# Kernel tuning notes

Hardware: AMD Instinct MI355X
Metric: run time of the kernel (lower is better)

Reference implementation:

```python
import jax, jax.numpy as jnp
import numpy as np

B, S, D, H = 4, 2048, 1024, 16
HD = D // H  # head dim = 64


def setup_inputs() -> dict:
    key = jax.random.key(0)
    k1, k2, k3 = jax.random.split(key, 3)
    scale = 1.0 / np.sqrt(D).astype(np.float32)
    x = jax.random.normal(k1, (B, S, D), dtype=jnp.float32)
    # q/k slices of nn.MultiheadAttention's in_proj (v and out_proj never
    # influence the returned values since x_t is discarded by forward)
    wq = jax.random.normal(k2, (D, D), dtype=jnp.float32) * scale
    wk = jax.random.normal(k3, (D, D), dtype=jnp.float32) * scale
    bq = jnp.zeros((D,), dtype=jnp.float32)
    bk = jnp.zeros((D,), dtype=jnp.float32)
    # 8 contiguous scale blocks of 256 tokens; last boundary == S
    scales_idx = (jnp.arange(1, 9, dtype=jnp.int64) * (S // 8))
    return {"x": x, "wq": wq, "wk": wk, "bq": bq, "bk": bk,
            "scales_idx": scales_idx}


def reference(x, wq, wk, bq, bk, scales_idx):
    b, s, d = x.shape
    # project q, k and split heads: [B, H, S, HD]
    q = (x @ wq.T + bq).reshape(b, s, H, HD).transpose(0, 2, 1, 3)
    k = (x @ wk.T + bk).reshape(b, s, H, HD).transpose(0, 2, 1, 3)
    inv_sqrt_hd = jnp.asarray(1.0 / np.sqrt(HD), dtype=x.dtype)
    scores = jnp.einsum('bhqd,bhkd->bhqk', q, k) * inv_sqrt_hd  # [B,H,S,S]
    # block-diagonal mask: token i belongs to the block whose right boundary
    # is the first scales_idx entry strictly greater than i
    pos = jnp.arange(s)
    seg = jnp.searchsorted(scales_idx, pos, side='right')  # [S]
    allowed = seg[:, None] == seg[None, :]                  # [S,S] bool
    scores = jnp.where(allowed[None, None], scores, -jnp.inf)
    w = jax.nn.softmax(scores, axis=-1)  # every row has >=1 allowed entry
    weights_attn = jnp.mean(w, axis=1)   # average over heads -> [B,S,S]
    return (x, weights_attn)
```

## Files before the change

### kernel.cpp

```cpp
#include <hip/hip_runtime.h>
#include <hip/hip_bf16.h>
#include <math.h>

#define BB 4
#define SS 2048
#define DD 1024
#define HH 16
#define HD 64
#define MM (BB*SS)
#define NN (2*DD)
#define BK 64
#define NKT 16

typedef __attribute__((ext_vector_type(8))) short short8;
typedef __attribute__((ext_vector_type(4))) float f32x4;
typedef unsigned short ushort_t;

__device__ __forceinline__ void gload16(const void* g, void* l) {
    __builtin_amdgcn_global_load_lds((const __attribute__((address_space(1))) unsigned int*)g,
                                     (__attribute__((address_space(3))) unsigned int*)l,
                                     16, 0, 0);
}

__global__ __launch_bounds__(256)
void copy_cast(const float* __restrict__ x, float* __restrict__ out_x,
               __hip_bfloat16* __restrict__ xb, int n8)
{
    int i = blockIdx.x * 256 + threadIdx.x;
    if (i >= n8) return;
    const f32x4* s = (const f32x4*)x + (size_t)i * 2;
    f32x4 a = s[0], b = s[1];
    f32x4* o = (f32x4*)out_x + (size_t)i * 2;
    __builtin_nontemporal_store(a, o);
    __builtin_nontemporal_store(b, o + 1);
    __hip_bfloat16 tmp[8];
    tmp[0] = __float2bfloat16(a.x); tmp[1] = __float2bfloat16(a.y);
    tmp[2] = __float2bfloat16(a.z); tmp[3] = __float2bfloat16(a.w);
    tmp[4] = __float2bfloat16(b.x); tmp[5] = __float2bfloat16(b.y);
    tmp[6] = __float2bfloat16(b.z); tmp[7] = __float2bfloat16(b.w);
    *(float4*)&xb[(size_t)i * 8] = *(float4*)tmp;
}

__global__ __launch_bounds__(256)
void cast_w(const float* __restrict__ wq, const float* __restrict__ wk,
            __hip_bfloat16* __restrict__ wb)
{
    const int half = (DD * DD) / 8;
    int i = blockIdx.x * 256 + threadIdx.x;
    if (i >= 2 * half) return;
    const float* src = (i < half) ? wq : wk;
    int j = (i < half) ? i : i - half;
    const float4* s = (const float4*)src + (size_t)j * 2;
    float4 a = s[0], b = s[1];
    __hip_bfloat16 tmp[8];
    tmp[0] = __float2bfloat16(a.x); tmp[1] = __float2bfloat16(a.y);
    tmp[2] = __float2bfloat16(a.z); tmp[3] = __float2bfloat16(a.w);
    tmp[4] = __float2bfloat16(b.x); tmp[5] = __float2bfloat16(b.y);
    tmp[6] = __float2bfloat16(b.z); tmp[7] = __float2bfloat16(b.w);
    *(float4*)&wb[(size_t)i * 8] = *(float4*)tmp;
}

__device__ __forceinline__ void stage_A(const ushort_t* __restrict__ xb, ushort_t* Ab,
                                        int m0, int kt, int mh, int wv, int lane)
{
    #pragma unroll
    for (int it = 0; it < 2; ++it) {
        int rl0 = it * 64 + wv * 8;
        int r0 = (rl0 & 63) + ((rl0 >> 6) << 7) + mh * 64;
        int r  = r0 + (lane >> 3);
        int gch = (lane & 7) ^ (r & 7);
        gload16(xb + (size_t)(m0 + r) * DD + kt + gch * 8, Ab + r0 * 64);
    }
}

__device__ __forceinline__ void stage_Bt(const ushort_t* __restrict__ wb, ushort_t* Bb,
                                         int n0, int kt, int nh, int wv, int lane)
{
    #pragma unroll
    for (int it = 0; it < 2; ++it) {
        int rl0 = it * 64 + wv * 8;
        int r0 = (rl0 & 31) + ((rl0 >> 5) << 6) + nh * 32;
        int r  = r0 + (lane >> 3);
        int gch = (lane & 7) ^ (r & 7);
        gload16(wb + (size_t)(n0 + r) * DD + kt + gch * 8, Bb + r0 * 64);
    }
}

__global__ __launch_bounds__(512, 2)
void proj_mfma(const ushort_t* __restrict__ xb, const ushort_t* __restrict__ wb,
               const float* __restrict__ bq, const float* __restrict__ bk,
               __hip_bfloat16* __restrict__ Qb, __hip_bfloat16* __restrict__ Kb)
{
    __shared__ __align__(16) ushort_t As[2][256 * BK];
    __shared__ __align__(16) ushort_t Bs[2][256 * BK];

    const int t = threadIdx.x;
    const int wv = t >> 6, lane = t & 63, quad = lane >> 4, l15 = lane & 15;
    const int wr = wv >> 2, wc = wv & 3;
    const int m0 = blockIdx.x * 256, n0 = blockIdx.y * 256;

    f32x4 acc[8][4];
    #pragma unroll
    for (int mt = 0; mt < 8; ++mt)
        #pragma unroll
        for (int nt = 0; nt < 4; ++nt) acc[mt][nt] = (f32x4){0.f, 0.f, 0.f, 0.f};

    stage_Bt(wb, Bs[0], n0, 0, 0, wv, lane);
    stage_A (xb, As[0], m0, 0, 0, wv, lane);
    stage_A (xb, As[0], m0, 0, 1, wv, lane);
    stage_Bt(wb, Bs[0], n0, 0, 1, wv, lane);
    stage_Bt(wb, Bs[1], n0, BK, 0, wv, lane);
    stage_A (xb, As[1], m0, BK, 0, wv, lane);
    asm volatile("s_waitcnt vmcnt(4)" ::: "memory");
    __builtin_amdgcn_s_barrier();

    #pragma unroll 1
    for (int tt = 0; tt < NKT; ++tt) {
        ushort_t* Ac = As[tt & 1];
        ushort_t* Bc = Bs[tt & 1];
        ushort_t* An = As[(tt & 1) ^ 1];
        ushort_t* Bn = Bs[(tt & 1) ^ 1];
        short8 a[8][2], b[2][2];

        #pragma unroll
        for (int mt = 0; mt < 4; ++mt)
            #pragma unroll
            for (int ks = 0; ks < 2; ++ks) {
                int r = wr * 128 + mt * 16 + l15;
                int sl = r * 8 + ((ks * 4 + quad) ^ (r & 7));
                a[mt][ks] = *(const short8*)&Ac[sl * 8];
            }
        #pragma unroll
        for (int nt = 0; nt < 2; ++nt)
            #pragma unroll
            for (int ks = 0; ks < 2; ++ks) {
                int r = wc * 64 + nt * 16 + l15;
                int sl = r * 8 + ((ks * 4 + quad) ^ (r & 7));
                b[nt][ks] = *(const short8*)&Bc[sl * 8];
            }
        if (tt + 1 < NKT) stage_A(xb, An, m0, (tt + 1) * BK, 1, wv, lane);
        __builtin_amdgcn_s_barrier();
        asm volatile("s_waitcnt lgkmcnt(0)" ::: "memory");
        __builtin_amdgcn_sched_barrier(0);
        __builtin_amdgcn_s_setprio(1);
        #pragma unroll
        for (int mt = 0; mt < 4; ++mt)
            #pragma unroll
            for (int nt = 0; nt < 2; ++nt)
                #pragma unroll
                for (int ks = 0; ks < 2; ++ks)
                    acc[mt][nt] = __builtin_amdgcn_mfma_f32_16x16x32_bf16(
                        a[mt][ks], b[nt][ks], acc[mt][nt], 0, 0, 0);
        __builtin_amdgcn_s_setprio(0);
        __builtin_amdgcn_sched_barrier(0);
        __builtin_amdgcn_s_barrier();

        #pragma unroll
        for (int mt = 0; mt < 4; ++mt)
            #pragma unroll
            for (int ks = 0; ks < 2; ++ks) {
                int r = wr * 128 + 64 + mt * 16 + l15;
                int sl = r * 8 + ((ks * 4 + quad) ^ (r & 7));
                a[4 + mt][ks] = *(const short8*)&Ac[sl * 8];
            }
        if (tt + 1 < NKT) stage_Bt(wb, Bn, n0, (tt + 1) * BK, 1, wv, lane);
        __builtin_amdgcn_s_barrier();
        asm volatile("s_waitcnt lgkmcnt(0)" ::: "memory");
        __builtin_amdgcn_sched_barrier(0);
        __builtin_amdgcn_s_setprio(1);
        #pragma unroll
        for (int mt = 0; mt < 4; ++mt)
            #pragma unroll
            for (int nt = 0; nt < 2; ++nt)
                #pragma unroll
                for (int ks = 0; ks < 2; ++ks)
                    acc[4 + mt][nt] = __builtin_amdgcn_mfma_f32_16x16x32_bf16(
                        a[4 + mt][ks], b[nt][ks], acc[4 + mt][nt], 0, 0, 0);
        __builtin_amdgcn_s_setprio(0);
        __builtin_amdgcn_sched_barrier(0);
        __builtin_amdgcn_s_barrier();

        #pragma unroll
        for (int nt = 0; nt < 2; ++nt)
            #pragma unroll
            for (int ks = 0; ks < 2; ++ks) {
                int r = wc * 64 + 32 + nt * 16 + l15;
                int sl = r * 8 + ((ks * 4 + quad) ^ (r & 7));
                b[nt][ks] = *(const short8*)&Bc[sl * 8];
            }
        if (tt + 2 < NKT) stage_Bt(wb, Bc, n0, (tt + 2) * BK, 0, wv, lane);
        __builtin_amdgcn_s_barrier();
        asm volatile("s_waitcnt lgkmcnt(0)" ::: "memory");
        __builtin_amdgcn_sched_barrier(0);
        __builtin_amdgcn_s_setprio(1);
        #pragma unroll
        for (int mt = 0; mt < 4; ++mt)
            #pragma unroll
            for (int nt = 0; nt < 2; ++nt)
                #pragma unroll
                for (int ks = 0; ks < 2; ++ks)
                    acc[mt][2 + nt] = __builtin_amdgcn_mfma_f32_16x16x32_bf16(
                        a[mt][ks], b[nt][ks], acc[mt][2 + nt], 0, 0, 0);
        __builtin_amdgcn_s_setprio(0);
        __builtin_amdgcn_sched_barrier(0);
        __builtin_amdgcn_s_barrier();

        if (tt + 2 < NKT) stage_A(xb, Ac, m0, (tt + 2) * BK, 0, wv, lane);
        __builtin_amdgcn_s_barrier();
        asm volatile("s_waitcnt lgkmcnt(0)" ::: "memory");
        __builtin_amdgcn_sched_barrier(0);
        __builtin_amdgcn_s_setprio(1);
        #pragma unroll
        for (int mt = 0; mt < 4; ++mt)
            #pragma unroll
            for (int nt = 0; nt < 2; ++nt)
                #pragma unroll
                for (int ks = 0; ks < 2; ++ks)
                    acc[4 + mt][2 + nt] = __builtin_amdgcn_mfma_f32_16x16x32_bf16(
                        a[4 + mt][ks], b[nt][ks], acc[4 + mt][2 + nt], 0, 0, 0);
        __builtin_amdgcn_s_setprio(0);
        __builtin_amdgcn_sched_barrier(0);
        if (tt < NKT - 2)       asm volatile("s_waitcnt vmcnt(4)" ::: "memory");
        else if (tt == NKT - 2) asm volatile("s_waitcnt vmcnt(0)" ::: "memory");
        __builtin_amdgcn_s_barrier();
    }

    const bool isQ = (n0 < DD);
    const float* bias = isQ ? bq : bk;
    __hip_bfloat16* outp = isQ ? Qb : Kb;
    const int nc0 = (isQ ? n0 : n0 - DD) + wc * 64;
    #pragma unroll
    for (int nt = 0; nt < 4; ++nt) {
        const int nc = nc0 + nt * 16 + l15;
        const float bv = bias[nc];
        #pragma unroll
        for (int mt = 0; mt < 8; ++mt)
            #pragma unroll
            for (int reg = 0; reg < 4; ++reg) {
                int m = m0 + wr * 128 + mt * 16 + quad * 4 + reg;
                outp[(size_t)m * DD + nc] = __float2bfloat16(acc[mt][nt][reg] + bv);
            }
    }
}

__global__ __launch_bounds__(256, 1)
void attn_block(const ushort_t* __restrict__ Qb, const ushort_t* __restrict__ Kb,
                const int* __restrict__ scales, float* __restrict__ outw)
{
    __shared__ __align__(16) char smem[147456];
    float (*comb)[256] = (float(*)[256])smem;

    const int bid = blockIdx.x;
    const int rt  = bid >> 5;
    const int blk = bid & 7, bb = (bid >> 3) & 3;
    const int start = blk ? scales[blk - 1] : 0;

    const int t = threadIdx.x;
    const int wv = t >> 6, lane = t & 63, quad = lane >> 4, l15 = lane & 15;
    const int rg = wv & 1, hg = wv >> 1;

    f32x4 accm[16];
    #pragma unroll
    for (int nt = 0; nt < 16; ++nt) accm[nt] = (f32x4){0.f, 0.f, 0.f, 0.f};

    const int qrow0 = start + rt * 32;
    const int brow  = bb * SS;

    auto stageKQ = [&](int i, int buf) {
        #pragma unroll
        for (int half = 0; half < 2; ++half) {
            const int h = half * 8 + i;
            ushort_t* Kl = (ushort_t*)(smem + (size_t)(buf * 2 + half) * 32768);
            ushort_t* Ql = (ushort_t*)(smem + 131072 + (size_t)(buf * 2 + half) * 4096);
            #pragma unroll
            for (int round = 0; round < 8; ++round) {
                int c = round * 256 + t;
                int row = c >> 3, ch = c & 7;
                int gch = ch ^ (row & 7);
                gload16(Kb + (size_t)(brow + start + row) * DD + h * HD + gch * 8,
                        Kl + ((size_t)round * 256 + wv * 64) * 8);
            }
            {
                int row = t >> 3, ch = t & 7;
                int gch = ch ^ (row & 7);
                gload16(Qb + (size_t)(brow + qrow0 + row) * DD + h * HD + gch * 8,
                        Ql + ((size_t)wv * 64) * 8);
            }
        }
    };

    stageKQ(0, 0);

    for (int i = 0; i < 8; ++i) {
        if (i < 7) {
            stageKQ(i + 1, (i + 1) & 1);
            asm volatile("s_waitcnt vmcnt(18)" ::: "memory");
        } else {
            asm volatile("s_waitcnt vmcnt(0)" ::: "memory");
        }
        __builtin_amdgcn_s_barrier();

        const ushort_t* Ks = (const ushort_t*)(smem + (size_t)((i & 1) * 2 + hg) * 32768);
        const ushort_t* Qs = (const ushort_t*)(smem + 131072 + (size_t)((i & 1) * 2 + hg) * 4096);

        short8 af[2];
        #pragma unroll
        for (int ks = 0; ks < 2; ++ks) {
            int qr = rg * 16 + l15;
            int sl = qr * 8 + ((ks * 4 + quad) ^ (qr & 7));
            af[ks] = *(const short8*)&Qs[sl * 8];
        }
        f32x4 sc[16];
        #pragma unroll
        for (int nt = 0; nt < 16; ++nt) {
            sc[nt] = (f32x4){0.f, 0.f, 0.f, 0.f};
            #pragma unroll
            for (int ks = 0; ks < 2; ++ks) {
                int kr = nt * 16 + l15;
                int sl = kr * 8 + ((ks * 4 + quad) ^ (kr & 7));
                short8 bf = *(const short8*)&Ks[sl * 8];
                sc[nt] = __builtin_amdgcn_mfma_f32_16x16x32_bf16(af[ks], bf, sc[nt], 0, 0, 0);
            }
        }
        float rs[4] = {0.f, 0.f, 0.f, 0.f};
        #pragma unroll
        for (int nt = 0; nt < 16; ++nt) {
            #pragma unroll
            for (int r = 0; r < 4; ++r) {
                float p = __expf(sc[nt][r] * 0.125f);
                sc[nt][r] = p;
                rs[r] += p;
            }
        }
        #pragma unroll
        for (int r = 0; r < 4; ++r) {
            #pragma unroll
            for (int off = 1; off < 16; off <<= 1) rs[r] += __shfl_xor(rs[r], off, 64);
            rs[r] = 1.0f / rs[r];
        }
        #pragma unroll
        for (int nt = 0; nt < 16; ++nt)
            #pragma unroll
            for (int r = 0; r < 4; ++r) accm[nt][r] += sc[nt][r] * rs[r];

        __builtin_amdgcn_s_barrier();
    }

    __syncthreads();
    if (hg == 0) {
        #pragma unroll
        for (int nt = 0; nt < 16; ++nt)
            #pragma unroll
            for (int r = 0; r < 4; ++r)
                comb[rg * 16 + quad * 4 + r][nt * 16 + l15] = accm[nt][r];
    }
    __syncthreads();
    if (hg == 1) {
        #pragma unroll
        for (int nt = 0; nt < 16; ++nt)
            #pragma unroll
            for (int r = 0; r < 4; ++r)
                comb[rg * 16 + quad * 4 + r][nt * 16 + l15] += accm[nt][r];
    }
    __syncthreads();

    const float s16 = 1.0f / (float)HH;
    const size_t orow0 = (size_t)bb * SS + qrow0;
    #pragma unroll
    for (int it = 0; it < 64; ++it) {
        int flat = it * 256 + t;
        int row = flat >> 9;
        int col = (flat & 511) * 4;
        f32x4 v = (f32x4){0.f, 0.f, 0.f, 0.f};
        unsigned lc = (unsigned)(col - start);
        if (lc < 256u) {
            const float* c = &comb[row][lc];
            v = (f32x4){c[0] * s16, c[1] * s16, c[2] * s16, c[3] * s16};
        }
        __builtin_nontemporal_store(v, (f32x4*)&outw[(orow0 + row) * SS + col]);
    }
}

extern "C" void kernel_launch(void* const* d_in, const int* in_sizes, int n_in,
                              void* d_out, int out_size, void* d_ws, size_t ws_size,
                              hipStream_t stream)
{
    const float* x  = (const float*)d_in[0];
    const float* wq = (const float*)d_in[1];
    const float* wk = (const float*)d_in[2];
    const float* bq = (const float*)d_in[3];
    const float* bk = (const float*)d_in[4];
    const int* scales = (const int*)d_in[5];

    float* out_x = (float*)d_out;
    float* out_w = out_x + (size_t)BB * SS * DD;

    char* w = (char*)d_ws;
    __hip_bfloat16* xb = (__hip_bfloat16*)(w);
    __hip_bfloat16* wb = (__hip_bfloat16*)(w + 16777216);
    __hip_bfloat16* Qb = (__hip_bfloat16*)(w + 20971520);
    __hip_bfloat16* Kb = (__hip_bfloat16*)(w + 37748736);

    copy_cast<<<4096, 256, 0, stream>>>(x, out_x, xb, (MM * DD) / 8);
    cast_w<<<1024, 256, 0, stream>>>(wq, wk, wb);

    dim3 pgrid(MM / 256, NN / 256);
    proj_mfma<<<pgrid, 512, 0, stream>>>((const ushort_t*)xb, (const ushort_t*)wb,
                                         bq, bk, Qb, Kb);

    attn_block<<<256, 256, 0, stream>>>((const ushort_t*)Qb, (const ushort_t*)Kb,
                                        scales, out_w);
}
```

Baseline: 208.0 us.

## Collapse four-phase GEMM main loop into two phases with fewer barriers

```diff
diff --git a/kernel.cpp b/kernel.cpp
--- a/kernel.cpp
+++ b/kernel.cpp
@@ -120,10 +120,10 @@
         ushort_t* Bc = Bs[tt & 1];
         ushort_t* An = As[(tt & 1) ^ 1];
         ushort_t* Bn = Bs[(tt & 1) ^ 1];
-        short8 a[8][2], b[2][2];
-
-        #pragma unroll
-        for (int mt = 0; mt < 4; ++mt)
+        short8 a[8][2], b0[2][2], b1[2][2];
+
+        #pragma unroll
+        for (int mt = 0; mt < 8; ++mt)
             #pragma unroll
             for (int ks = 0; ks < 2; ++ks) {
                 int r = wr * 128 + mt * 16 + l15;
@@ -136,88 +136,51 @@
             for (int ks = 0; ks < 2; ++ks) {
                 int r = wc * 64 + nt * 16 + l15;
                 int sl = r * 8 + ((ks * 4 + quad) ^ (r & 7));
-                b[nt][ks] = *(const short8*)&Bc[sl * 8];
-            }
-        if (tt + 1 < NKT) stage_A(xb, An, m0, (tt + 1) * BK, 1, wv, lane);
+                b0[nt][ks] = *(const short8*)&Bc[sl * 8];
+            }
+        if (tt + 1 < NKT) {
+            stage_A (xb, An, m0, (tt + 1) * BK, 1, wv, lane);
+            stage_Bt(wb, Bn, n0, (tt + 1) * BK, 1, wv, lane);
+        }
         __builtin_amdgcn_s_barrier();
         asm volatile("s_waitcnt lgkmcnt(0)" ::: "memory");
         __builtin_amdgcn_sched_barrier(0);
         __builtin_amdgcn_s_setprio(1);
         #pragma unroll
-        for (int mt = 0; mt < 4; ++mt)
+        for (int mt = 0; mt < 8; ++mt)
             #pragma unroll
             for (int nt = 0; nt < 2; ++nt)
                 #pragma unroll
                 for (int ks = 0; ks < 2; ++ks)
                     acc[mt][nt] = __builtin_amdgcn_mfma_f32_16x16x32_bf16(
-                        a[mt][ks], b[nt][ks], acc[mt][nt], 0, 0, 0);
+                        a[mt][ks], b0[nt][ks], acc[mt][nt], 0, 0, 0);
         __builtin_amdgcn_s_setprio(0);
         __builtin_amdgcn_sched_barrier(0);
         __builtin_amdgcn_s_barrier();
 
         #pragma unroll
-        for (int mt = 0; mt < 4; ++mt)
+        for (int nt = 0; nt < 2; ++nt)
             #pragma unroll
             for (int ks = 0; ks < 2; ++ks) {
-                int r = wr * 128 + 64 + mt * 16 + l15;
+                int r = wc * 64 + 32 + nt * 16 + l15;
                 int sl = r * 8 + ((ks * 4 + quad) ^ (r & 7));
-                a[4 + mt][ks] = *(const short8*)&Ac[sl * 8];
-            }
-        if (tt + 1 < NKT) stage_Bt(wb, Bn, n0, (tt + 1) * BK, 1, wv, lane);
-        __builtin_amdgcn_s_barrier();
+                b1[nt][ks] = *(const short8*)&Bc[sl * 8];
+            }
+        if (tt + 2 < NKT) {
+            stage_Bt(wb, Bc, n0, (tt + 2) * BK, 0, wv, lane);
+            stage_A (xb, Ac, m0, (tt + 2) * BK, 0, wv, lane);
+        }
         asm volatile("s_waitcnt lgkmcnt(0)" ::: "memory");
         __builtin_amdgcn_sched_barrier(0);
         __builtin_amdgcn_s_setprio(1);
         #pragma unroll
-        for (int mt = 0; mt < 4; ++mt)
-            #pragma unroll
-            for (int nt = 0; nt < 2; ++nt)
-                #pragma unroll
-                for (int ks = 0; ks < 2; ++ks)
-                    acc[4 + mt][nt] = __builtin_amdgcn_mfma_f32_16x16x32_bf16(
-                        a[4 + mt][ks], b[nt][ks], acc[4 + mt][nt], 0, 0, 0);
-        __builtin_amdgcn_s_setprio(0);
-        __builtin_amdgcn_sched_barrier(0);
-        __builtin_amdgcn_s_barrier();
-
-        #pragma unroll
-        for (int nt = 0; nt < 2; ++nt)
-            #pragma unroll
-            for (int ks = 0; ks < 2; ++ks) {
-                int r = wc * 64 + 32 + nt * 16 + l15;
-                int sl = r * 8 + ((ks * 4 + quad) ^ (r & 7));
-                b[nt][ks] = *(const short8*)&Bc[sl * 8];
-            }
-        if (tt + 2 < NKT) stage_Bt(wb, Bc, n0, (tt + 2) * BK, 0, wv, lane);
-        __builtin_amdgcn_s_barrier();
-        asm volatile("s_waitcnt lgkmcnt(0)" ::: "memory");
-        __builtin_amdgcn_sched_barrier(0);
-        __builtin_amdgcn_s_setprio(1);
-        #pragma unroll
-        for (int mt = 0; mt < 4; ++mt)
+        for (int mt = 0; mt < 8; ++mt)
             #pragma unroll
             for (int nt = 0; nt < 2; ++nt)
                 #pragma unroll
                 for (int ks = 0; ks < 2; ++ks)
                     acc[mt][2 + nt] = __builtin_amdgcn_mfma_f32_16x16x32_bf16(
-                        a[mt][ks], b[nt][ks], acc[mt][2 + nt], 0, 0, 0);
-        __builtin_amdgcn_s_setprio(0);
-        __builtin_amdgcn_sched_barrier(0);
-        __builtin_amdgcn_s_barrier();
-
-        if (tt + 2 < NKT) stage_A(xb, Ac, m0, (tt + 2) * BK, 0, wv, lane);
-        __builtin_amdgcn_s_barrier();
-        asm volatile("s_waitcnt lgkmcnt(0)" ::: "memory");
-        __builtin_amdgcn_sched_barrier(0);
-        __builtin_amdgcn_s_setprio(1);
-        #pragma unroll
-        for (int mt = 0; mt < 4; ++mt)
-            #pragma unroll
-            for (int nt = 0; nt < 2; ++nt)
-                #pragma unroll
-                for (int ks = 0; ks < 2; ++ks)
-                    acc[4 + mt][2 + nt] = __builtin_amdgcn_mfma_f32_16x16x32_bf16(
-                        a[4 + mt][ks], b[nt][ks], acc[4 + mt][2 + nt], 0, 0, 0);
+                        a[mt][ks], b1[nt][ks], acc[mt][2 + nt], 0, 0, 0);
         __builtin_amdgcn_s_setprio(0);
         __builtin_amdgcn_sched_barrier(0);
         if (tt < NKT - 2)       asm volatile("s_waitcnt vmcnt(4)" ::: "memory");
```

After: 205.1 us, median of 2. About the same (-1.4%).
